# Optimization experiments

Hardware: AMD Instinct MI355X
Metric: run time of the kernel (lower is better)

Reference implementation:

```python
import jax, jax.numpy as jnp
import numpy as np
from jax import lax

B, T, V, D, K = 64, 512, 32000, 768, 29

def setup_inputs() -> dict:
    key = jax.random.key(0)
    ks = jax.random.split(key, 8)
    x = jax.random.randint(ks[0], (B, T), 0, V)
    tags = jax.random.randint(ks[1], (B, T), 0, K)
    emb = jax.random.normal(ks[2], (V, D), dtype=jnp.float32) * 0.02
    w = jax.random.normal(ks[3], (K, D), dtype=jnp.float32) * 0.02
    b = jnp.zeros((K,), dtype=jnp.float32)
    start_trans = jax.random.normal(ks[4], (K,), dtype=jnp.float32) * 0.1
    end_trans = jax.random.normal(ks[5], (K,), dtype=jnp.float32) * 0.1
    trans = jax.random.normal(ks[6], (K, K), dtype=jnp.float32) * 0.1
    return {"x": x, "tags": tags, "emb": emb, "w": w, "b": b,
            "start_trans": start_trans, "end_trans": end_trans, "trans": trans}

def _emissions(x, emb, w, b):
    e = emb[x]                                   # [B,T,D] (dropout is identity at inference)
    return jnp.einsum('btd,kd->btk', e, w) + b   # [B,T,K]

def _crf_nll(em, tags, start_trans, end_trans, trans):
    # numerator: score of the gold tag path (full mask)
    num = start_trans[tags[:, 0]]
    num = num + jnp.take_along_axis(em[:, 0], tags[:, 0:1], axis=1)[:, 0]
    num = num + jnp.sum(trans[tags[:, :-1], tags[:, 1:]], axis=1)
    num = num + jnp.sum(jnp.take_along_axis(em[:, 1:], tags[:, 1:, None], axis=2)[..., 0], axis=1)
    num = num + end_trans[tags[:, -1]]
    # denominator: forward algorithm (log partition)
    def step(alpha, e_t):
        # alpha [B,K] prev-tag scores; e_t [B,K] current emissions
        nxt = jax.nn.logsumexp(alpha[:, :, None] + trans[None], axis=1) + e_t
        return nxt, None
    alpha0 = start_trans[None] + em[:, 0]
    alpha, _ = lax.scan(step, alpha0, jnp.swapaxes(em[:, 1:], 0, 1))
    logZ = jax.nn.logsumexp(alpha + end_trans[None], axis=1)
    return -jnp.sum(num - logZ)  # torchcrf default reduction='sum', model negates

def _viterbi(em, start_trans, end_trans, trans):
    def vstep(score, e_t):
        cand = score[:, :, None] + trans[None]   # [B,K_prev,K_cur]
        bp = jnp.argmax(cand, axis=1)            # [B,K]
        return jnp.max(cand, axis=1) + e_t, bp
    score0 = start_trans[None] + em[:, 0]
    score, bps = lax.scan(vstep, score0, jnp.swapaxes(em[:, 1:], 0, 1))  # bps [T-1,B,K]
    last = jnp.argmax(score + end_trans[None], axis=1)                   # [B]
    def back(tag, bp):
        prev = jnp.take_along_axis(bp, tag[:, None], axis=1)[:, 0]
        return prev, prev
    _, path = lax.scan(back, last, bps, reverse=True)                    # [T-1,B], tags 0..T-2
    return jnp.concatenate([jnp.swapaxes(path, 0, 1), last[:, None]], axis=1)

def reference(x, tags, emb, w, b, start_trans, end_trans, trans):
    em = _emissions(x, emb, w, b)
    nll = _crf_nll(em, tags, start_trans, end_trans, trans)
    decoded = _viterbi(em, start_trans, end_trans, trans)
    return nll, decoded
```

## Files before the change

kernel.cpp:

```cpp
#include <hip/hip_runtime.h>
#include <math.h>

#define NB 64
#define NT 512
#define ND 768
#define NK 29
#define L2E 1.4426950408889634f
#define LN2 0.6931471805599453f
#define NEG_BIG -1e30f

typedef __attribute__((ext_vector_type(8))) short short8;
typedef __attribute__((ext_vector_type(4))) float floatx4;

__device__ __forceinline__ short bf16r(float f) {
    unsigned u = __float_as_uint(f);
    unsigned r = (u + 0x7FFFu + ((u >> 16) & 1u)) >> 16;
    return (short)r;
}

__global__ __launch_bounds__(256) void k_prep(const float* __restrict__ w,
                                              short* __restrict__ wbf)
{
    int i = blockIdx.x * 256 + threadIdx.x;
    if (i < 32 * ND) {
        int row = i / ND;
        wbf[i] = (row < NK) ? bf16r(w[i]) : (short)0;
    }
}

__global__ __launch_bounds__(128) void k_emissions(
    const int* __restrict__ x, const float* __restrict__ emb,
    const short* __restrict__ wbf, const float* __restrict__ bias,
    float* __restrict__ em)
{
    __shared__ float red[2 * 256];
    const int lane = threadIdx.x & 63;
    const int wv = threadIdx.x >> 6;
    const int col = lane & 15;
    const int quad = lane >> 4;
    const int Mbase = blockIdx.x * 16;
    const int tok = Mbase + col;

    const float* arow = emb + (size_t)x[tok] * ND + wv * 384 + quad * 8;
    const short* brow0 = wbf + (size_t)col * ND + wv * 384 + quad * 8;
    const short* brow1 = brow0 + 16 * ND;

    floatx4 acc0 = {0.f, 0.f, 0.f, 0.f};
    floatx4 acc1 = {0.f, 0.f, 0.f, 0.f};

    float4 a0  = *(const float4*)(arow);
    float4 a0b = *(const float4*)(arow + 4);
    float4 a1  = *(const float4*)(arow + 32);
    float4 a1b = *(const float4*)(arow + 36);
    short8 b0  = *(const short8*)(brow0);
    short8 b1  = *(const short8*)(brow1);

    for (int c = 0; c < 12; ++c) {
        int c2 = (c + 2 <= 11) ? c + 2 : 11;
        float4 n0  = *(const float4*)(arow + c2 * 32);
        float4 n0b = *(const float4*)(arow + c2 * 32 + 4);
        int c1 = (c + 1 <= 11) ? c + 1 : 11;
        short8 nb0 = *(const short8*)(brow0 + c1 * 32);
        short8 nb1 = *(const short8*)(brow1 + c1 * 32);

        short8 af;
        af[0] = bf16r(a0.x);  af[1] = bf16r(a0.y);
        af[2] = bf16r(a0.z);  af[3] = bf16r(a0.w);
        af[4] = bf16r(a0b.x); af[5] = bf16r(a0b.y);
        af[6] = bf16r(a0b.z); af[7] = bf16r(a0b.w);

        acc0 = __builtin_amdgcn_mfma_f32_16x16x32_bf16(af, b0, acc0, 0, 0, 0);
        acc1 = __builtin_amdgcn_mfma_f32_16x16x32_bf16(af, b1, acc1, 0, 0, 0);

        a0 = a1; a0b = a1b; a1 = n0; a1b = n0b;
        b0 = nb0; b1 = nb1;
    }

    const int r0 = quad * 4;
    if (wv == 1) {
#pragma unroll
        for (int reg = 0; reg < 4; ++reg) {
            red[(r0 + reg) * 16 + col]       = acc0[reg];
            red[256 + (r0 + reg) * 16 + col] = acc1[reg];
        }
    }
    __syncthreads();
    if (wv == 0) {
        float bs0 = bias[col];
        float bs1 = (col < NK - 16) ? bias[16 + col] : 0.f;
#pragma unroll
        for (int reg = 0; reg < 4; ++reg) {
            int row = r0 + reg;
            float v0 = acc0[reg] + red[row * 16 + col] + bs0;
            em[(size_t)(Mbase + row) * NK + col] = v0;
            if (col < NK - 16) {
                float v1 = acc1[reg] + red[256 + row * 16 + col] + bs1;
                em[(size_t)(Mbase + row) * NK + 16 + col] = v1;
            }
        }
    }
}

__global__ __launch_bounds__(64) void k_scan(
    const float* __restrict__ em, const int* __restrict__ tags,
    const float* __restrict__ st, const float* __restrict__ en,
    const float* __restrict__ tr, float* __restrict__ part,
    float* __restrict__ out)
{
    __shared__ __align__(16) float sA[32];
    __shared__ __align__(16) unsigned char smem[NT * NK * 4];
    const float4* sA4 = (const float4*)sA;
    const int lane = threadIdx.x;
    const int jc = (lane < NK) ? lane : NK - 1;

    if (blockIdx.x < NB) {
        const int b = blockIdx.x;
        float* emS = (float*)smem;
        {
            const float4* src = (const float4*)(em + (size_t)b * NT * NK);
            float4* dst = (float4*)emS;
            for (int i = lane; i < NT * NK / 4; i += 64) dst[i] = src[i];
        }
        float EC[32];
#pragma unroll
        for (int i = 0; i < NK; ++i) EC[i] = __expf(tr[i * NK + jc]);
#pragma unroll
        for (int i = NK; i < 32; ++i) EC[i] = 0.f;

        float a0v = __expf(st[jc] + emS[jc]);
        if (lane < 32) sA[lane] = (lane < NK) ? a0v : 0.f;

        int eshift = 5 * (NT - 1);
        float eemc = exp2f(fmaf(emS[NK + jc], L2E, -5.0f));
        float rawn = emS[2 * NK + jc];
        float anew = a0v;

        for (int t = 1; t < NT; ++t) {
            float4 A[8];
#pragma unroll
            for (int ii = 0; ii < 8; ++ii) A[ii] = sA4[ii];
            float p0 = 0.f, p1 = 0.f, p2 = 0.f, p3 = 0.f;
#pragma unroll
            for (int ii = 0; ii < 8; ++ii) {
                p0 = fmaf(A[ii].x, EC[4 * ii + 0], p0);
                p1 = fmaf(A[ii].y, EC[4 * ii + 1], p1);
                p2 = fmaf(A[ii].z, EC[4 * ii + 2], p2);
                p3 = fmaf(A[ii].w, EC[4 * ii + 3], p3);
            }
            anew = ((p0 + p1) + (p2 + p3)) * eemc;
            eemc = exp2f(fmaf(rawn, L2E, -5.0f));
            int tn = t + 2; tn = tn < NT ? tn : NT - 1;
            rawn = emS[tn * NK + jc];

            if ((t & 15) == 0) {
                unsigned mb = (unsigned)__builtin_amdgcn_readfirstlane(
                                  __float_as_int(anew));
                int ex = (int)((mb >> 23) & 255u) - 127;
                anew *= __int_as_float((unsigned)(127 - ex) << 23);
                eshift += ex;
            }
            if (lane < 32) sA[lane] = (lane < NK) ? anew : 0.f;
        }
        float val = (lane < NK) ? anew * __expf(en[jc]) : 0.f;
#pragma unroll
        for (int s = 32; s; s >>= 1) val += __shfl_xor(val, s);
        float logZ = logf(val) + (float)eshift * LN2;
        const int* tg = tags + b * NT;
        float p = 0.f;
        for (int t = lane; t < NT; t += 64) {
            int tt = tg[t];
            p += emS[t * NK + tt];
            if (t == 0) p += st[tt];
            else        p += tr[tg[t - 1] * NK + tt];
            if (t == NT - 1) p += en[tt];
        }
#pragma unroll
        for (int s = 32; s; s >>= 1) p += __shfl_xor(p, s);
        if (lane == 0) part[b] = logZ - p;
    } else {
        const int b = blockIdx.x - NB;
        const float* emb_b = em + (size_t)b * NT * NK;
        unsigned char* sbp = smem;
        unsigned char* smap = smem + 511 * 32;

        float Tc[32];
#pragma unroll
        for (int i = 0; i < NK; ++i) Tc[i] = tr[i * NK + jc];
#pragma unroll
        for (int i = NK; i < 32; ++i) Tc[i] = 0.f;

        float sc = (lane < NK) ? (st[jc] + emb_b[jc]) : NEG_BIG;
        if (lane < 32) sA[lane] = (lane < NK) ? sc : NEG_BIG;

        float e0 = emb_b[1 * NK + jc];
        float e1 = emb_b[2 * NK + jc];
        float e2 = emb_b[3 * NK + jc];
        float e3 = emb_b[4 * NK + jc];

        auto vstep = [&](int t, float emt) {
            float4 q[8];
#pragma unroll
            for (int ii = 0; ii < 8; ++ii) q[ii] = sA4[ii];
            float v[32]; int id[32];
#pragma unroll
            for (int ii = 0; ii < 8; ++ii) {
                v[4 * ii + 0] = q[ii].x + Tc[4 * ii + 0];
                v[4 * ii + 1] = q[ii].y + Tc[4 * ii + 1];
                v[4 * ii + 2] = q[ii].z + Tc[4 * ii + 2];
                v[4 * ii + 3] = q[ii].w + Tc[4 * ii + 3];
            }
#pragma unroll
            for (int i = 0; i < 32; ++i) id[i] = i;
#pragma unroll
            for (int w2 = 16; w2 >= 1; w2 >>= 1)
#pragma unroll
                for (int i = 0; i < 16; ++i) {
                    if (i < w2) {
                        bool g = v[i + w2] > v[i];
                        v[i] = g ? v[i + w2] : v[i];
                        id[i] = g ? id[i + w2] : id[i];
                    }
                }
            if (lane < 32) sbp[(t - 1) * 32 + lane] = (unsigned char)id[0];
            sc = (lane < NK) ? (v[0] + emt) : NEG_BIG;
            if (lane < 32) sA[lane] = (lane < NK) ? sc : NEG_BIG;
        };

        int t = 1;
        for (; t + 3 < NT; t += 4) {
            vstep(t + 0, e0); { int tn = t + 4; tn = tn < NT ? tn : NT - 1; e0 = emb_b[tn * NK + jc]; }
            vstep(t + 1, e1); { int tn = t + 5; tn = tn < NT ? tn : NT - 1; e1 = emb_b[tn * NK + jc]; }
            vstep(t + 2, e2); { int tn = t + 6; tn = tn < NT ? tn : NT - 1; e2 = emb_b[tn * NK + jc]; }
            vstep(t + 3, e3); { int tn = t + 7; tn = tn < NT ? tn : NT - 1; e3 = emb_b[tn * NK + jc]; }
        }
        vstep(509, e0); vstep(510, e1); vstep(511, e2);

        float v = (lane < NK) ? (sc + en[jc]) : NEG_BIG;
        float M = v;
#pragma unroll
        for (int s = 32; s; s >>= 1) M = fmaxf(M, __shfl_xor(M, s));
        unsigned long long mk = __ballot((lane < NK) && v == M);
        int last = (int)__builtin_ctzll(mk);

        const int h = lane >> 5, j5 = lane & 31;
        int cur8[8];
#pragma unroll
        for (int rep = 0; rep < 8; ++rep) cur8[rep] = j5;
        for (int off = 0; off < 32; ++off) {
#pragma unroll
            for (int rep = 0; rep < 8; ++rep) {
                int s = 2 * rep + h;
                int hi = (s == 15) ? 511 : 32 * s + 32;
                int r = hi - 1 - off;
                if (r >= 32 * s) cur8[rep] = sbp[r * 32 + cur8[rep]];
            }
        }
#pragma unroll
        for (int rep = 0; rep < 8; ++rep)
            smap[(2 * rep + h) * 32 + j5] = (unsigned char)cur8[rep];

        int myhi = 0, cur = last;
        for (int s = 15; s >= 0; --s) {
            if (lane == s) myhi = cur;
            cur = smap[s * 32 + cur];
        }
        float* op = out + 1 + (size_t)b * NT;
        if (lane == 16) op[NT - 1] = (float)last;
        if (lane < 16) {
            int s = lane;
            int hi = (s == 15) ? 511 : 32 * s + 32;
            int c = myhi;
            for (int r = hi - 1; r >= 32 * s; --r) {
                c = sbp[r * 32 + c];
                op[r] = (float)c;
            }
        }
    }
}

__global__ __launch_bounds__(64) void k_finish(const float* __restrict__ part,
                                               float* __restrict__ out)
{
    float v = part[threadIdx.x];
#pragma unroll
    for (int s = 32; s; s >>= 1) v += __shfl_xor(v, s);
    if (threadIdx.x == 0) out[0] = v;
}

extern "C" void kernel_launch(void* const* d_in, const int* in_sizes, int n_in,
                              void* d_out, int out_size, void* d_ws, size_t ws_size,
                              hipStream_t stream) {
    const int*   x    = (const int*)d_in[0];
    const int*   tags = (const int*)d_in[1];
    const float* emb  = (const float*)d_in[2];
    const float* w    = (const float*)d_in[3];
    const float* bias = (const float*)d_in[4];
    const float* st   = (const float*)d_in[5];
    const float* en   = (const float*)d_in[6];
    const float* tr   = (const float*)d_in[7];
    float* out = (float*)d_out;

    short* wbf  = (short*)d_ws;
    float* part = (float*)((char*)d_ws + 49152);
    float* em   = (float*)((char*)d_ws + 65536);

    k_prep<<<96, 256, 0, stream>>>(w, wbf);
    k_emissions<<<2048, 128, 0, stream>>>(x, emb, wbf, bias, em);
    k_scan<<<2 * NB, 64, 0, stream>>>(em, tags, st, en, tr, part, out);
    k_finish<<<1, 64, 0, stream>>>(part, out);
}
```

Measured before the change: 349.7 us.

## Split CRF scan reductions across wave halves and preload emission rows

The forward and Viterbi recurrences now split the 32 previous-tag terms between the two 32-lane halves of the wavefront. Each half reduces 16 terms and the partial results are combined with permlane32_swap, so each lane's serial step chain is roughly halved. Viterbi tie-breaking keeps the lowest index so the argmax matches the reference. The emissions kernel also loads all 24 float4 chunks of each embedding row up front, fully unrolls the MFMA loop and adds an occupancy hint to launch_bounds. This trades higher register pressure for more memory parallelism.

```diff
diff --git a/kernel.cpp b/kernel.cpp
--- a/kernel.cpp
+++ b/kernel.cpp
@@ -11,11 +11,25 @@
 
 typedef __attribute__((ext_vector_type(8))) short short8;
 typedef __attribute__((ext_vector_type(4))) float floatx4;
+typedef __attribute__((ext_vector_type(2))) unsigned u32x2;
 
 __device__ __forceinline__ short bf16r(float f) {
     unsigned u = __float_as_uint(f);
     unsigned r = (u + 0x7FFFu + ((u >> 16) & 1u)) >> 16;
     return (short)r;
+}
+
+__device__ __forceinline__ void swap32f(float x, float& a, float& b) {
+    u32x2 r = __builtin_amdgcn_permlane32_swap(__float_as_uint(x),
+                                               __float_as_uint(x), false, false);
+    a = __uint_as_float(r[0]);
+    b = __uint_as_float(r[1]);
+}
+__device__ __forceinline__ void swap32i(int x, int& a, int& b) {
+    u32x2 r = __builtin_amdgcn_permlane32_swap((unsigned)x, (unsigned)x,
+                                               false, false);
+    a = (int)r[0];
+    b = (int)r[1];
 }
 
 __global__ __launch_bounds__(256) void k_prep(const float* __restrict__ w,
@@ -28,7 +42,7 @@
     }
 }
 
-__global__ __launch_bounds__(128) void k_emissions(
+__global__ __launch_bounds__(128, 3) void k_emissions(
     const int* __restrict__ x, const float* __restrict__ emb,
     const short* __restrict__ wbf, const float* __restrict__ bias,
     float* __restrict__ em)
@@ -45,34 +59,34 @@
     const short* brow0 = wbf + (size_t)col * ND + wv * 384 + quad * 8;
     const short* brow1 = brow0 + 16 * ND;
 
+    float4 a[24];
+#pragma unroll
+    for (int c = 0; c < 12; ++c) {
+        a[2 * c]     = *(const float4*)(arow + c * 32);
+        a[2 * c + 1] = *(const float4*)(arow + c * 32 + 4);
+    }
+
     floatx4 acc0 = {0.f, 0.f, 0.f, 0.f};
     floatx4 acc1 = {0.f, 0.f, 0.f, 0.f};
 
-    float4 a0  = *(const float4*)(arow);
-    float4 a0b = *(const float4*)(arow + 4);
-    float4 a1  = *(const float4*)(arow + 32);
-    float4 a1b = *(const float4*)(arow + 36);
-    short8 b0  = *(const short8*)(brow0);
-    short8 b1  = *(const short8*)(brow1);
-
+    short8 b0 = *(const short8*)(brow0);
+    short8 b1 = *(const short8*)(brow1);
+
+#pragma unroll
     for (int c = 0; c < 12; ++c) {
-        int c2 = (c + 2 <= 11) ? c + 2 : 11;
-        float4 n0  = *(const float4*)(arow + c2 * 32);
-        float4 n0b = *(const float4*)(arow + c2 * 32 + 4);
         int c1 = (c + 1 <= 11) ? c + 1 : 11;
         short8 nb0 = *(const short8*)(brow0 + c1 * 32);
         short8 nb1 = *(const short8*)(brow1 + c1 * 32);
 
         short8 af;
-        af[0] = bf16r(a0.x);  af[1] = bf16r(a0.y);
-        af[2] = bf16r(a0.z);  af[3] = bf16r(a0.w);
-        af[4] = bf16r(a0b.x); af[5] = bf16r(a0b.y);
-        af[6] = bf16r(a0b.z); af[7] = bf16r(a0b.w);
+        af[0] = bf16r(a[2 * c].x);     af[1] = bf16r(a[2 * c].y);
+        af[2] = bf16r(a[2 * c].z);     af[3] = bf16r(a[2 * c].w);
+        af[4] = bf16r(a[2 * c + 1].x); af[5] = bf16r(a[2 * c + 1].y);
+        af[6] = bf16r(a[2 * c + 1].z); af[7] = bf16r(a[2 * c + 1].w);
 
         acc0 = __builtin_amdgcn_mfma_f32_16x16x32_bf16(af, b0, acc0, 0, 0, 0);
         acc1 = __builtin_amdgcn_mfma_f32_16x16x32_bf16(af, b1, acc1, 0, 0, 0);
 
-        a0 = a1; a0b = a1b; a1 = n0; a1b = n0b;
         b0 = nb0; b1 = nb1;
     }
 
@@ -109,9 +123,11 @@
 {
     __shared__ __align__(16) float sA[32];
     __shared__ __align__(16) unsigned char smem[NT * NK * 4];
-    const float4* sA4 = (const float4*)sA;
     const int lane = threadIdx.x;
-    const int jc = (lane < NK) ? lane : NK - 1;
+    const int c = lane & 31;
+    const int h = lane >> 5;
+    const int jc = (c < NK) ? c : NK - 1;
+    const float4* sAh = (const float4*)(sA + 16 * h);
 
     if (blockIdx.x < NB) {
         const int b = blockIdx.x;
@@ -121,11 +137,12 @@
             float4* dst = (float4*)emS;
             for (int i = lane; i < NT * NK / 4; i += 64) dst[i] = src[i];
         }
-        float EC[32];
-#pragma unroll
-        for (int i = 0; i < NK; ++i) EC[i] = __expf(tr[i * NK + jc]);
-#pragma unroll
-        for (int i = NK; i < 32; ++i) EC[i] = 0.f;
+        float ECh[16];
+#pragma unroll
+        for (int r = 0; r < 16; ++r) {
+            int i = 16 * h + r;
+            ECh[r] = (i < NK) ? __expf(tr[i * NK + jc]) : 0.f;
+        }
 
         float a0v = __expf(st[jc] + emS[jc]);
         if (lane < 32) sA[lane] = (lane < NK) ? a0v : 0.f;
@@ -136,18 +153,20 @@
         float anew = a0v;
 
         for (int t = 1; t < NT; ++t) {
-            float4 A[8];
-#pragma unroll
-            for (int ii = 0; ii < 8; ++ii) A[ii] = sA4[ii];
+            float4 A0 = sAh[0], A1 = sAh[1], A2 = sAh[2], A3 = sAh[3];
             float p0 = 0.f, p1 = 0.f, p2 = 0.f, p3 = 0.f;
-#pragma unroll
-            for (int ii = 0; ii < 8; ++ii) {
-                p0 = fmaf(A[ii].x, EC[4 * ii + 0], p0);
-                p1 = fmaf(A[ii].y, EC[4 * ii + 1], p1);
-                p2 = fmaf(A[ii].z, EC[4 * ii + 2], p2);
-                p3 = fmaf(A[ii].w, EC[4 * ii + 3], p3);
-            }
-            anew = ((p0 + p1) + (p2 + p3)) * eemc;
+            p0 = fmaf(A0.x, ECh[0], p0);  p1 = fmaf(A0.y, ECh[1], p1);
+            p2 = fmaf(A0.z, ECh[2], p2);  p3 = fmaf(A0.w, ECh[3], p3);
+            p0 = fmaf(A1.x, ECh[4], p0);  p1 = fmaf(A1.y, ECh[5], p1);
+            p2 = fmaf(A1.z, ECh[6], p2);  p3 = fmaf(A1.w, ECh[7], p3);
+            p0 = fmaf(A2.x, ECh[8], p0);  p1 = fmaf(A2.y, ECh[9], p1);
+            p2 = fmaf(A2.z, ECh[10], p2); p3 = fmaf(A2.w, ECh[11], p3);
+            p0 = fmaf(A3.x, ECh[12], p0); p1 = fmaf(A3.y, ECh[13], p1);
+            p2 = fmaf(A3.z, ECh[14], p2); p3 = fmaf(A3.w, ECh[15], p3);
+            float ph = (p0 + p1) + (p2 + p3);
+            float plo, phi;
+            swap32f(ph, plo, phi);
+            anew = (plo + phi) * eemc;
             eemc = exp2f(fmaf(rawn, L2E, -5.0f));
             int tn = t + 2; tn = tn < NT ? tn : NT - 1;
             rawn = emS[tn * NK + jc];
@@ -183,14 +202,17 @@
         unsigned char* sbp = smem;
         unsigned char* smap = smem + 511 * 32;
 
-        float Tc[32];
-#pragma unroll
-        for (int i = 0; i < NK; ++i) Tc[i] = tr[i * NK + jc];
-#pragma unroll
-        for (int i = NK; i < 32; ++i) Tc[i] = 0.f;
-
-        float sc = (lane < NK) ? (st[jc] + emb_b[jc]) : NEG_BIG;
-        if (lane < 32) sA[lane] = (lane < NK) ? sc : NEG_BIG;
+        float Tch[16];
+        int idA[16];
+#pragma unroll
+        for (int r = 0; r < 16; ++r) {
+            int i = 16 * h + r;
+            Tch[r] = (i < NK) ? tr[i * NK + jc] : 0.f;
+            idA[r] = i;
+        }
+
+        float sc = (c < NK) ? (st[jc] + emb_b[jc]) : NEG_BIG;
+        if (lane < 32) sA[lane] = (c < NK) ? sc : NEG_BIG;
 
         float e0 = emb_b[1 * NK + jc];
         float e1 = emb_b[2 * NK + jc];
@@ -198,32 +220,40 @@
         float e3 = emb_b[4 * NK + jc];
 
         auto vstep = [&](int t, float emt) {
-            float4 q[8];
-#pragma unroll
-            for (int ii = 0; ii < 8; ++ii) q[ii] = sA4[ii];
-            float v[32]; int id[32];
-#pragma unroll
-            for (int ii = 0; ii < 8; ++ii) {
-                v[4 * ii + 0] = q[ii].x + Tc[4 * ii + 0];
-                v[4 * ii + 1] = q[ii].y + Tc[4 * ii + 1];
-                v[4 * ii + 2] = q[ii].z + Tc[4 * ii + 2];
-                v[4 * ii + 3] = q[ii].w + Tc[4 * ii + 3];
-            }
-#pragma unroll
-            for (int i = 0; i < 32; ++i) id[i] = i;
-#pragma unroll
-            for (int w2 = 16; w2 >= 1; w2 >>= 1)
-#pragma unroll
-                for (int i = 0; i < 16; ++i) {
-                    if (i < w2) {
-                        bool g = v[i + w2] > v[i];
-                        v[i] = g ? v[i + w2] : v[i];
-                        id[i] = g ? id[i + w2] : id[i];
-                    }
+            float4 q0 = sAh[0], q1 = sAh[1], q2 = sAh[2], q3 = sAh[3];
+            float v[16];
+            v[0]  = q0.x + Tch[0];  v[1]  = q0.y + Tch[1];
+            v[2]  = q0.z + Tch[2];  v[3]  = q0.w + Tch[3];
+            v[4]  = q1.x + Tch[4];  v[5]  = q1.y + Tch[5];
+            v[6]  = q1.z + Tch[6];  v[7]  = q1.w + Tch[7];
+            v[8]  = q2.x + Tch[8];  v[9]  = q2.y + Tch[9];
+            v[10] = q2.z + Tch[10]; v[11] = q2.w + Tch[11];
+            v[12] = q3.x + Tch[12]; v[13] = q3.y + Tch[13];
+            v[14] = q3.z + Tch[14]; v[15] = q3.w + Tch[15];
+            int id[16];
+#pragma unroll
+            for (int i = 0; i < 16; i += 2) {
+                bool g = v[i + 1] > v[i];
+                v[i]  = g ? v[i + 1] : v[i];
+                id[i] = g ? idA[i + 1] : idA[i];
+            }
+#pragma unroll
+            for (int s = 2; s < 16; s <<= 1)
+#pragma unroll
+                for (int i = 0; i < 16; i += 2 * s) {
+                    bool g = v[i + s] > v[i];
+                    v[i]  = g ? v[i + s] : v[i];
+                    id[i] = g ? id[i + s] : id[i];
                 }
-            if (lane < 32) sbp[(t - 1) * 32 + lane] = (unsigned char)id[0];
-            sc = (lane < NK) ? (v[0] + emt) : NEG_BIG;
-            if (lane < 32) sA[lane] = (lane < NK) ? sc : NEG_BIG;
+            float va, vb; int ia, ib;
+            swap32f(v[0], va, vb);
+            swap32i(id[0], ia, ib);
+            bool bb = (vb > va) || (vb == va && ib < ia);
+            float bw = bb ? vb : va;
+            int   bi = bb ? ib : ia;
+            if (lane < 32) sbp[(t - 1) * 32 + lane] = (unsigned char)bi;
+            sc = bw + emt;
+            if (lane < 32) sA[lane] = (c < NK) ? sc : NEG_BIG;
         };
 
         int t = 1;
@@ -235,17 +265,16 @@
         }
         vstep(509, e0); vstep(510, e1); vstep(511, e2);
 
-        float v = (lane < NK) ? (sc + en[jc]) : NEG_BIG;
-        float M = v;
+        float vfin = (lane < NK) ? (sc + en[jc]) : NEG_BIG;
+        float M = vfin;
 #pragma unroll
         for (int s = 32; s; s >>= 1) M = fmaxf(M, __shfl_xor(M, s));
-        unsigned long long mk = __ballot((lane < NK) && v == M);
+        unsigned long long mk = __ballot((lane < NK) && vfin == M);
         int last = (int)__builtin_ctzll(mk);
 
-        const int h = lane >> 5, j5 = lane & 31;
         int cur8[8];
 #pragma unroll
-        for (int rep = 0; rep < 8; ++rep) cur8[rep] = j5;
+        for (int rep = 0; rep < 8; ++rep) cur8[rep] = c;
         for (int off = 0; off < 32; ++off) {
 #pragma unroll
             for (int rep = 0; rep < 8; ++rep) {
@@ -257,7 +286,7 @@
         }
 #pragma unroll
         for (int rep = 0; rep < 8; ++rep)
-            smap[(2 * rep + h) * 32 + j5] = (unsigned char)cur8[rep];
+            smap[(2 * rep + h) * 32 + c] = (unsigned char)cur8[rep];
 
         int myhi = 0, cur = last;
         for (int s = 15; s >= 0; --s) {
@@ -269,10 +298,10 @@
         if (lane < 16) {
             int s = lane;
             int hi = (s == 15) ? 511 : 32 * s + 32;
-            int c = myhi;
+            int cc = myhi;
             for (int r = hi - 1; r >= 32 * s; --r) {
-                c = sbp[r * 32 + c];
-                op[r] = (float)c;
+                cc = sbp[r * 32 + cc];
+                op[r] = (float)cc;
             }
         }
     }
```

Result: faster. 311.6 us (-10.9%).

## Broadcast scan state via readlane instead of LDS round-trip; preload embedding rows

Applied to the files above, without the earlier changes.

The serial forward and Viterbi recurrences no longer write the per-tag state to shared memory and read it back each step. Each lane's state now stays in a register and is broadcast to the whole wave with 32 readlane calls, removing an LDS store/load round-trip from the critical dependency chain of the 511-step loops. Separately, the emissions kernel issues all 12 embedding-row loads up front into a 24-entry register array and fully unrolls the MFMA loop. This raises register pressure in exchange for more memory-level parallelism. Readlane produces scalar values, which may add SGPR-to-VGPR moves per step.

```diff
diff --git a/kernel.cpp b/kernel.cpp
--- a/kernel.cpp
+++ b/kernel.cpp
@@ -16,6 +16,10 @@
     unsigned u = __float_as_uint(f);
     unsigned r = (u + 0x7FFFu + ((u >> 16) & 1u)) >> 16;
     return (short)r;
+}
+
+__device__ __forceinline__ float rlane(float v, int i) {
+    return __int_as_float(__builtin_amdgcn_readlane(__float_as_int(v), i));
 }
 
 __global__ __launch_bounds__(256) void k_prep(const float* __restrict__ w,
@@ -45,34 +49,34 @@
     const short* brow0 = wbf + (size_t)col * ND + wv * 384 + quad * 8;
     const short* brow1 = brow0 + 16 * ND;
 
+    float4 a[24];
+#pragma unroll
+    for (int c = 0; c < 12; ++c) {
+        a[2 * c]     = *(const float4*)(arow + c * 32);
+        a[2 * c + 1] = *(const float4*)(arow + c * 32 + 4);
+    }
+
     floatx4 acc0 = {0.f, 0.f, 0.f, 0.f};
     floatx4 acc1 = {0.f, 0.f, 0.f, 0.f};
 
-    float4 a0  = *(const float4*)(arow);
-    float4 a0b = *(const float4*)(arow + 4);
-    float4 a1  = *(const float4*)(arow + 32);
-    float4 a1b = *(const float4*)(arow + 36);
-    short8 b0  = *(const short8*)(brow0);
-    short8 b1  = *(const short8*)(brow1);
-
+    short8 b0 = *(const short8*)(brow0);
+    short8 b1 = *(const short8*)(brow1);
+
+#pragma unroll
     for (int c = 0; c < 12; ++c) {
-        int c2 = (c + 2 <= 11) ? c + 2 : 11;
-        float4 n0  = *(const float4*)(arow + c2 * 32);
-        float4 n0b = *(const float4*)(arow + c2 * 32 + 4);
         int c1 = (c + 1 <= 11) ? c + 1 : 11;
         short8 nb0 = *(const short8*)(brow0 + c1 * 32);
         short8 nb1 = *(const short8*)(brow1 + c1 * 32);
 
         short8 af;
-        af[0] = bf16r(a0.x);  af[1] = bf16r(a0.y);
-        af[2] = bf16r(a0.z);  af[3] = bf16r(a0.w);
-        af[4] = bf16r(a0b.x); af[5] = bf16r(a0b.y);
-        af[6] = bf16r(a0b.z); af[7] = bf16r(a0b.w);
+        af[0] = bf16r(a[2 * c].x);     af[1] = bf16r(a[2 * c].y);
+        af[2] = bf16r(a[2 * c].z);     af[3] = bf16r(a[2 * c].w);
+        af[4] = bf16r(a[2 * c + 1].x); af[5] = bf16r(a[2 * c + 1].y);
+        af[6] = bf16r(a[2 * c + 1].z); af[7] = bf16r(a[2 * c + 1].w);
 
         acc0 = __builtin_amdgcn_mfma_f32_16x16x32_bf16(af, b0, acc0, 0, 0, 0);
         acc1 = __builtin_amdgcn_mfma_f32_16x16x32_bf16(af, b1, acc1, 0, 0, 0);
 
-        a0 = a1; a0b = a1b; a1 = n0; a1b = n0b;
         b0 = nb0; b1 = nb1;
     }
 
@@ -107,11 +111,10 @@
     const float* __restrict__ tr, float* __restrict__ part,
     float* __restrict__ out)
 {
-    __shared__ __align__(16) float sA[32];
     __shared__ __align__(16) unsigned char smem[NT * NK * 4];
-    const float4* sA4 = (const float4*)sA;
     const int lane = threadIdx.x;
-    const int jc = (lane < NK) ? lane : NK - 1;
+    const int c = lane & 31;
+    const int jc = (c < NK) ? c : NK - 1;
 
     if (blockIdx.x < NB) {
         const int b = blockIdx.x;
@@ -127,25 +130,24 @@
 #pragma unroll
         for (int i = NK; i < 32; ++i) EC[i] = 0.f;
 
-        float a0v = __expf(st[jc] + emS[jc]);
-        if (lane < 32) sA[lane] = (lane < NK) ? a0v : 0.f;
+        float anew = __expf(st[jc] + emS[jc]);
 
         int eshift = 5 * (NT - 1);
         float eemc = exp2f(fmaf(emS[NK + jc], L2E, -5.0f));
         float rawn = emS[2 * NK + jc];
-        float anew = a0v;
 
         for (int t = 1; t < NT; ++t) {
-            float4 A[8];
-#pragma unroll
-            for (int ii = 0; ii < 8; ++ii) A[ii] = sA4[ii];
+            float curm = (c < NK) ? anew : 0.f;
+            float S[32];
+#pragma unroll
+            for (int i = 0; i < 32; ++i) S[i] = rlane(curm, i);
             float p0 = 0.f, p1 = 0.f, p2 = 0.f, p3 = 0.f;
 #pragma unroll
             for (int ii = 0; ii < 8; ++ii) {
-                p0 = fmaf(A[ii].x, EC[4 * ii + 0], p0);
-                p1 = fmaf(A[ii].y, EC[4 * ii + 1], p1);
-                p2 = fmaf(A[ii].z, EC[4 * ii + 2], p2);
-                p3 = fmaf(A[ii].w, EC[4 * ii + 3], p3);
+                p0 = fmaf(S[4 * ii + 0], EC[4 * ii + 0], p0);
+                p1 = fmaf(S[4 * ii + 1], EC[4 * ii + 1], p1);
+                p2 = fmaf(S[4 * ii + 2], EC[4 * ii + 2], p2);
+                p3 = fmaf(S[4 * ii + 3], EC[4 * ii + 3], p3);
             }
             anew = ((p0 + p1) + (p2 + p3)) * eemc;
             eemc = exp2f(fmaf(rawn, L2E, -5.0f));
@@ -159,7 +161,6 @@
                 anew *= __int_as_float((unsigned)(127 - ex) << 23);
                 eshift += ex;
             }
-            if (lane < 32) sA[lane] = (lane < NK) ? anew : 0.f;
         }
         float val = (lane < NK) ? anew * __expf(en[jc]) : 0.f;
 #pragma unroll
@@ -189,8 +190,7 @@
 #pragma unroll
         for (int i = NK; i < 32; ++i) Tc[i] = 0.f;
 
-        float sc = (lane < NK) ? (st[jc] + emb_b[jc]) : NEG_BIG;
-        if (lane < 32) sA[lane] = (lane < NK) ? sc : NEG_BIG;
+        float sc = (c < NK) ? (st[jc] + emb_b[jc]) : NEG_BIG;
 
         float e0 = emb_b[1 * NK + jc];
         float e1 = emb_b[2 * NK + jc];
@@ -198,19 +198,12 @@
         float e3 = emb_b[4 * NK + jc];
 
         auto vstep = [&](int t, float emt) {
-            float4 q[8];
-#pragma unroll
-            for (int ii = 0; ii < 8; ++ii) q[ii] = sA4[ii];
+            float S[32];
+#pragma unroll
+            for (int i = 0; i < 32; ++i) S[i] = rlane(sc, i);
             float v[32]; int id[32];
 #pragma unroll
-            for (int ii = 0; ii < 8; ++ii) {
-                v[4 * ii + 0] = q[ii].x + Tc[4 * ii + 0];
-                v[4 * ii + 1] = q[ii].y + Tc[4 * ii + 1];
-                v[4 * ii + 2] = q[ii].z + Tc[4 * ii + 2];
-                v[4 * ii + 3] = q[ii].w + Tc[4 * ii + 3];
-            }
-#pragma unroll
-            for (int i = 0; i < 32; ++i) id[i] = i;
+            for (int i = 0; i < 32; ++i) { v[i] = S[i] + Tc[i]; id[i] = i; }
 #pragma unroll
             for (int w2 = 16; w2 >= 1; w2 >>= 1)
 #pragma unroll
@@ -222,8 +215,7 @@
                     }
                 }
             if (lane < 32) sbp[(t - 1) * 32 + lane] = (unsigned char)id[0];
-            sc = (lane < NK) ? (v[0] + emt) : NEG_BIG;
-            if (lane < 32) sA[lane] = (lane < NK) ? sc : NEG_BIG;
+            sc = (c < NK) ? (v[0] + emt) : NEG_BIG;
         };
 
         int t = 1;
@@ -235,17 +227,17 @@
         }
         vstep(509, e0); vstep(510, e1); vstep(511, e2);
 
-        float v = (lane < NK) ? (sc + en[jc]) : NEG_BIG;
-        float M = v;
+        float vfin = (lane < NK) ? (sc + en[jc]) : NEG_BIG;
+        float M = vfin;
 #pragma unroll
         for (int s = 32; s; s >>= 1) M = fmaxf(M, __shfl_xor(M, s));
-        unsigned long long mk = __ballot((lane < NK) && v == M);
+        unsigned long long mk = __ballot((lane < NK) && vfin == M);
         int last = (int)__builtin_ctzll(mk);
 
-        const int h = lane >> 5, j5 = lane & 31;
+        const int h = lane >> 5;
         int cur8[8];
 #pragma unroll
-        for (int rep = 0; rep < 8; ++rep) cur8[rep] = j5;
+        for (int rep = 0; rep < 8; ++rep) cur8[rep] = c;
         for (int off = 0; off < 32; ++off) {
 #pragma unroll
             for (int rep = 0; rep < 8; ++rep) {
@@ -257,7 +249,7 @@
         }
 #pragma unroll
         for (int rep = 0; rep < 8; ++rep)
-            smap[(2 * rep + h) * 32 + j5] = (unsigned char)cur8[rep];
+            smap[(2 * rep + h) * 32 + c] = (unsigned char)cur8[rep];
 
         int myhi = 0, cur = last;
         for (int s = 15; s >= 0; --s) {
@@ -269,10 +261,10 @@
         if (lane < 16) {
             int s = lane;
             int hi = (s == 15) ? 511 : 32 * s + 32;
-            int c = myhi;
+            int cc = myhi;
             for (int r = hi - 1; r >= 32 * s; --r) {
-                c = sbp[r * 32 + c];
-                op[r] = (float)c;
+                cc = sbp[r * 32 + cc];
+                op[r] = (float)cc;
             }
         }
     }
```

New measurement: 343.1 us. About the same (-1.9%).
